# Kernel tuning notes

Measured on AMD Instinct MI355X. Metric: run time of the kernel, lower is better.

The kernel has to match this reference:

```python
import jax, jax.numpy as jnp
from jax import lax
import numpy as np

B, T, H, V, C = 64, 64, 1024, 32000, 10
Z, CD = 32, 8  # latent dim, cond embedding dim


def lstm_scan(x_tbh, h0, c0, Wih, Whh, bih, bhh):
    """PyTorch-convention LSTM over time. x_tbh: [T,B,H]; returns hs [T,B,H]."""
    def step(carry, x):
        h, c = carry
        gates = x @ Wih.T + bih + h @ Whh.T + bhh  # [B,4H]
        i, f, g, o = jnp.split(gates, 4, axis=-1)
        c = jax.nn.sigmoid(f) * c + jax.nn.sigmoid(i) * jnp.tanh(g)
        h = jax.nn.sigmoid(o) * jnp.tanh(c)
        return (h, c), h
    _, hs = lax.scan(step, (h0, c0), x_tbh)
    return hs


def setup_inputs() -> dict:
    key = jax.random.key(0)
    ks = jax.random.split(key, 24)
    s = 0.02
    d = {
        'input_word': jax.random.randint(ks[0], (B, T), 0, V),
        'cond': jax.random.randint(ks[1], (B,), 0, C),
        'emb_N': jax.random.normal(ks[2], (V, H), jnp.float32) * s,
        'Wih_N': jax.random.normal(ks[3], (4 * H, H), jnp.float32) * s,
        'Whh_N': jax.random.normal(ks[4], (4 * H, H), jnp.float32) * s,
        'bih_N': jnp.zeros((4 * H,), jnp.float32),
        'bhh_N': jnp.zeros((4 * H,), jnp.float32),
        'emb_D': jax.random.normal(ks[5], (V, H), jnp.float32) * s,
        'Wih_D': jax.random.normal(ks[6], (4 * H, H), jnp.float32) * s,
        'Whh_D': jax.random.normal(ks[7], (4 * H, H), jnp.float32) * s,
        'bih_D': jnp.zeros((4 * H,), jnp.float32),
        'bhh_D': jnp.zeros((4 * H,), jnp.float32),
        'emb_cond': jax.random.normal(ks[8], (C, CD), jnp.float32) * s,
        'W_mean': jax.random.normal(ks[9], (Z, H), jnp.float32) * s,
        'b_mean': jnp.zeros((Z,), jnp.float32),
        'W_logvar': jax.random.normal(ks[10], (Z, H), jnp.float32) * s,
        'b_logvar': jnp.zeros((Z,), jnp.float32),
        'W_st': jax.random.normal(ks[11], (H, Z + CD), jnp.float32) * s,
        'b_st': jnp.zeros((H,), jnp.float32),
        'W_out': jax.random.normal(ks[12], (V, H), jnp.float32) * s,
        'b_out': jnp.zeros((V,), jnp.float32),
        'eps': jax.random.normal(ks[13], (B, Z), jnp.float32),
    }
    return d


def reference(input_word, cond, emb_N, Wih_N, Whh_N, bih_N, bhh_N,
              emb_D, Wih_D, Whh_D, bih_D, bhh_D, emb_cond,
              W_mean, b_mean, W_logvar, b_logvar, W_st, b_st,
              W_out, b_out, eps):
    cond_e = emb_cond[cond]                              # [B,8]
    # ---- encoder ----
    x_enc = jnp.transpose(emb_N[input_word], (1, 0, 2))  # [T,B,H]
    h0 = jnp.concatenate([jnp.zeros((B, H - CD), x_enc.dtype), cond_e], axis=-1)
    c0 = jnp.zeros((B, H), x_enc.dtype)
    hs = lstm_scan(x_enc, h0, c0, Wih_N, Whh_N, bih_N, bhh_N)
    h_t = hs[-1]                                         # [B,H]
    mean_h = h_t @ W_mean.T + b_mean                     # [B,32]
    logvar_h = h_t @ W_logvar.T + b_logvar               # [B,32]
    latent_h = eps * jnp.exp(0.5 * logvar_h) + mean_h    # reparameterize
    # ---- decoder (teacher forcing, start token 0) ----
    hd0 = jnp.concatenate([latent_h, cond_e], axis=-1) @ W_st.T + b_st  # [B,H]
    cd0 = jnp.zeros((B, H), hd0.dtype)
    dec_tok = jnp.concatenate(
        [jnp.zeros((B, 1), input_word.dtype), input_word[:, :-1]], axis=1)
    x_dec = jnp.transpose(emb_D[dec_tok], (1, 0, 2))     # [T,B,H]
    hs_d = lstm_scan(x_dec, hd0, cd0, Wih_D, Whh_D, bih_D, bhh_D)  # [T,B,H]
    logits = hs_d @ W_out.T + b_out                      # [T,B,V]
    return jnp.transpose(logits, (1, 0, 2))              # [B,T,V]
```

## Files before the change

kernel.cpp:

```cpp
#include <hip/hip_runtime.h>
#include <hip/hip_bf16.h>

typedef unsigned short u16;
typedef unsigned int   u32;
typedef unsigned long long u64;
typedef __attribute__((ext_vector_type(8))) short short8;
typedef __attribute__((ext_vector_type(4))) float f32x4;

#define DEVINL static __device__ __forceinline__

DEVINL u16 f2bf(float x) {
  u32 u = __float_as_uint(x);
  u32 r = (u + 0x7fffu + ((u >> 16) & 1u)) >> 16;
  return (u16)r;
}

#define GLD16(gp, lp) __builtin_amdgcn_global_load_lds(                     \
    (const __attribute__((address_space(1))) u32*)(gp),                     \
    (__attribute__((address_space(3))) u32*)(lp), 16, 0, 0)

__global__ __launch_bounds__(256) void conv4(
    const float* __restrict__ s0, u16* __restrict__ d0,
    const float* __restrict__ s1, u16* __restrict__ d1,
    const float* __restrict__ s2, u16* __restrict__ d2,
    const float* __restrict__ s3, u16* __restrict__ d3) {
  int blk = blockIdx.x;
  int p = blk >> 12, local = blk & 4095;
  const float* s = (p == 0) ? s0 : (p == 1) ? s1 : (p == 2) ? s2 : s3;
  u16*         d = (p == 0) ? d0 : (p == 1) ? d1 : (p == 2) ? d2 : d3;
  int i = local * 256 + threadIdx.x;
  float4 v = ((const float4*)s)[i];
  ushort4 o;
  o.x = f2bf(v.x); o.y = f2bf(v.y); o.z = f2bf(v.z); o.w = f2bf(v.w);
  ((ushort4*)d)[i] = o;
}

__global__ __launch_bounds__(256) void conv_wout(const float* __restrict__ s,
                                                 u16* __restrict__ d) {
  int i = blockIdx.x * 256 + threadIdx.x;
  float4 v = ((const float4*)s)[i];
  ushort4 o;
  o.x = f2bf(v.x); o.y = f2bf(v.y); o.z = f2bf(v.z); o.w = f2bf(v.w);
  ((ushort4*)d)[i] = o;
}

__global__ __launch_bounds__(256) void prep_small(
    const int* __restrict__ cond, const float* __restrict__ emb_cond,
    const float* __restrict__ bihN, const float* __restrict__ bhhN,
    const float* __restrict__ bihD, const float* __restrict__ bhhD,
    float* __restrict__ ce, float* __restrict__ biasN, float* __restrict__ biasD,
    u32* __restrict__ bar) {
  int tid = blockIdx.x * 256 + threadIdx.x;
  if (tid < 512) {
    int b = tid >> 3, j = tid & 7;
    ce[tid] = emb_cond[cond[b] * 8 + j];
  }
  int i = tid - 512;
  if (i >= 0 && i < 4096) {
    biasN[i] = bihN[i] + bhhN[i];
    biasD[i] = bihD[i] + bhhD[i];
  }
  int k = tid - 4608;
  if (k >= 0 && k < 1024) bar[k] = 0;
}

__global__ __launch_bounds__(256) void init_enc(const float* __restrict__ ce,
                                                u16* __restrict__ hb0) {
  int tid = blockIdx.x * 256 + threadIdx.x;
  int b = tid >> 10, col = tid & 1023;
  float v = (col >= 1016) ? ce[b * 8 + (col - 1016)] : 0.f;
  hb0[tid] = f2bf(v);
}

__global__ __launch_bounds__(256) void gather_kernel(const float* __restrict__ emb,
                                                     const int* __restrict__ words,
                                                     u16* __restrict__ X, int dec) {
  int r = blockIdx.x;
  int t = r >> 6, b = r & 63;
  int tok = dec ? ((t == 0) ? 0 : words[b * 64 + t - 1]) : words[b * 64 + t];
  float4 v = ((const float4*)(emb + (size_t)tok * 1024))[threadIdx.x];
  ushort4 o;
  o.x = f2bf(v.x); o.y = f2bf(v.y); o.z = f2bf(v.z); o.w = f2bf(v.w);
  ((ushort4*)(X + (size_t)r * 1024))[threadIdx.x] = o;
}

DEVINL void gemm0_body(char* smemc, int bid, int nwg,
                       const u16* __restrict__ A, const u16* __restrict__ B,
                       float* __restrict__ C, const float* __restrict__ bias,
                       int N, int K) {
  u16 (*lA)[256 * 32] = (u16(*)[256 * 32])smemc;
  u16 (*lB)[128 * 32] = (u16(*)[128 * 32])(smemc + 32768);
  const int tid = threadIdx.x;
  const int lane = tid & 63;
  const int wid = tid >> 6;

  const int nn = N >> 7;
  const int wgid = (bid & 7) * (nwg >> 3) + (bid >> 3);
  const int tile_m = (wgid / nn) * 256;
  const int tile_n = (wgid % nn) * 128;
  const int wm = wid >> 1, wn = wid & 1;

  const int ldr = lane >> 2;
  const int lko = (lane & 3) * 8;
  const int l15 = lane & 15;
  const int g4 = lane >> 4;

  const size_t aBase = (size_t)tile_m * K;
  const size_t bBase = (size_t)tile_n * K;

  auto stage = [&](int buf, int k0) {
#pragma unroll
    for (int q = 0; q < 2; ++q) {
      int chk = wid * 2 + q;
      int row = chk * 16 + ldr;
      GLD16(A + aBase + (size_t)row * K + k0 + lko, &lA[buf][chk * 512]);
    }
    int row = wid * 16 + ldr;
    GLD16(B + bBase + (size_t)row * K + k0 + lko, &lB[buf][wid * 512]);
  };

  f32x4 acc[4][4];
#pragma unroll
  for (int i = 0; i < 4; ++i)
#pragma unroll
    for (int j = 0; j < 4; ++j) acc[i][j] = (f32x4)0.f;

  stage(0, 0);
  __syncthreads();

  const int NIT = K >> 5;
  for (int it = 0; it < NIT; ++it) {
    const int cur = it & 1;
    if (it + 1 < NIT) stage(cur ^ 1, (it + 1) * 32);
    short8 af[4], bf[4];
#pragma unroll
    for (int i = 0; i < 4; ++i)
      af[i] = *(const short8*)&lA[cur][(wm * 64 + i * 16 + l15) * 32 + g4 * 8];
#pragma unroll
    for (int j = 0; j < 4; ++j)
      bf[j] = *(const short8*)&lB[cur][(wn * 64 + j * 16 + l15) * 32 + g4 * 8];
#pragma unroll
    for (int i = 0; i < 4; ++i)
#pragma unroll
      for (int j = 0; j < 4; ++j)
        acc[i][j] = __builtin_amdgcn_mfma_f32_16x16x32_bf16(af[i], bf[j], acc[i][j], 0, 0, 0);
    __syncthreads();
  }

#pragma unroll
  for (int i = 0; i < 4; ++i) {
    int row0 = tile_m + wm * 64 + i * 16 + (g4 << 2);
#pragma unroll
    for (int j = 0; j < 4; ++j) {
      int col = tile_n + wn * 64 + j * 16 + l15;
      float bv = bias[col];
#pragma unroll
      for (int e = 0; e < 4; ++e)
        C[(size_t)(row0 + e) * (size_t)N + col] = acc[i][j][e] + bv;
    }
  }
}

DEVINL void lstm_body(char* smemc, const u16* __restrict__ Whh,
                      const float* __restrict__ Xp, u16* __restrict__ hbuf,
                      u16* __restrict__ hs_out, float* __restrict__ hT_out,
                      u32* arrive, u32* prog, int wgi) {
  char* smemA = smemc;
  float (*lg)[16][16] = (float(*)[16][16])(smemc + 32768);
  const int tid = threadIdx.x;
  const int lane = tid & 63;
  const int v = tid >> 6;
  const int gate = v >> 1;
  const int ch = v & 1;
  const int c = wgi >> 5;
  const int j = wgi & 31;
  const int b0 = c * 16, col0 = j * 32;
  const int l15 = lane & 15, g4 = lane >> 4;

  short8 breg[32];
  {
    const u16* Brow = Whh + (size_t)(gate * 1024 + col0 + ch * 16 + l15) * 1024
                          + g4 * 8;
#pragma unroll
    for (int kk = 0; kk < 32; ++kk)
      breg[kk] = *(const short8*)(Brow + kk * 32);
  }

  const int crow = tid >> 5, colw = tid & 31;
  const int bg = b0 + crow, cgl = col0 + colw;
  const int ch2 = colw >> 4, cw = colw & 15;
  float creg = 0.f;

  float xg0, xg1, xg2, xg3;
  {
    size_t xrow = (size_t)bg * 4096 + cgl;
    xg0 = __builtin_nontemporal_load(&Xp[xrow]);
    xg1 = __builtin_nontemporal_load(&Xp[xrow + 1024]);
    xg2 = __builtin_nontemporal_load(&Xp[xrow + 2048]);
    xg3 = __builtin_nontemporal_load(&Xp[xrow + 3072]);
  }

  for (int t = 0; t < 64; ++t) {
    const char* rbase = (const char*)(hbuf + (size_t)(t & 1) * 65536)
                      + (size_t)b0 * 2048;
    u32* wb32 = (u32*)(hbuf + (size_t)((t + 1) & 1) * 65536);

#pragma unroll
    for (int q = 0; q < 4; ++q) {
      int g = q * 512 + tid;
      int row = g >> 7;
      int cb = (g & 127) * 16;
      const u64* src = (const u64*)(rbase + (size_t)row * 2048 + cb);
      u64 lo = __hip_atomic_load(src,     __ATOMIC_RELAXED, __HIP_MEMORY_SCOPE_AGENT);
      u64 hi = __hip_atomic_load(src + 1, __ATOMIC_RELAXED, __HIP_MEMORY_SCOPE_AGENT);
      u64* d = (u64*)(smemA + row * 2048 + (cb ^ ((row & 7) << 4)));
      d[0] = lo; d[1] = hi;
    }
    __syncthreads();

    f32x4 a4[4] = {(f32x4)0.f, (f32x4)0.f, (f32x4)0.f, (f32x4)0.f};
#pragma unroll
    for (int kk = 0; kk < 32; ++kk) {
      int cb2 = kk * 64 + g4 * 16;
      const short8 a = *(const short8*)(smemA + l15 * 2048 + (cb2 ^ ((l15 & 7) << 4)));
      a4[kk & 3] = __builtin_amdgcn_mfma_f32_16x16x32_bf16(a, breg[kk], a4[kk & 3], 0, 0, 0);
    }
    f32x4 asum = a4[0] + a4[1] + a4[2] + a4[3];
    {
      int m = g4 * 4;
#pragma unroll
      for (int e = 0; e < 4; ++e) lg[v][m + e][l15] = asum[e];
    }
    __syncthreads();

    {
      float gi = lg[0 + ch2][crow][cw] + xg0;
      float gf = lg[2 + ch2][crow][cw] + xg1;
      float gg = lg[4 + ch2][crow][cw] + xg2;
      float go = lg[6 + ch2][crow][cw] + xg3;
      float si = 1.f / (1.f + __expf(-gi));
      float sf = 1.f / (1.f + __expf(-gf));
      float so = 1.f / (1.f + __expf(-go));
      float tg = tanhf(gg);
      float cn = sf * creg + si * tg;
      float hn = so * tanhf(cn);
      creg = cn;
      u16 h16 = f2bf(hn);
      u32 mine = h16;
      u32 other = (u32)__shfl_xor((int)mine, 1);
      if (!(colw & 1)) {
        u32 pk = mine | (other << 16);
        __hip_atomic_store(wb32 + (((size_t)bg * 1024 + cgl) >> 1), pk,
                           __ATOMIC_RELAXED, __HIP_MEMORY_SCOPE_AGENT);
        if (hs_out)
          __hip_atomic_store((u32*)hs_out + ((((size_t)t * 64 + bg) * 1024 + cgl) >> 1),
                             pk, __ATOMIC_RELAXED, __HIP_MEMORY_SCOPE_AGENT);
      }
      if (hT_out && t == 63) hT_out[bg * 1024 + cgl] = hn;
    }

    if (t != 63) {
      {
        size_t xrow = (size_t)((t + 1) * 64 + bg) * 4096 + cgl;
        xg0 = __builtin_nontemporal_load(&Xp[xrow]);
        xg1 = __builtin_nontemporal_load(&Xp[xrow + 1024]);
        xg2 = __builtin_nontemporal_load(&Xp[xrow + 2048]);
        xg3 = __builtin_nontemporal_load(&Xp[xrow + 3072]);
      }
      u32 want = (u32)(t + 1);
      asm volatile("s_waitcnt vmcnt(0)" ::: "memory");
      __syncthreads();
      if (tid == 0)
        __hip_atomic_store(&arrive[wgi], want, __ATOMIC_RELAXED,
                           __HIP_MEMORY_SCOPE_AGENT);
      if (tid < 32) {
        int guard = 0;
        while (__hip_atomic_load(&arrive[c * 32 + tid], __ATOMIC_RELAXED,
                                 __HIP_MEMORY_SCOPE_AGENT) < want) {
          __builtin_amdgcn_s_sleep(2);
          if (++guard > (1 << 20)) break;
        }
      }
      __syncthreads();
      if (prog && j == 0 && tid == 0)
        __hip_atomic_store(&prog[c], want, __ATOMIC_RELAXED,
                           __HIP_MEMORY_SCOPE_AGENT);
    }
  }

  if (prog) {
    asm volatile("s_waitcnt vmcnt(0)" ::: "memory");
    __syncthreads();
    if (tid == 0)
      __hip_atomic_store(&arrive[wgi], 64u, __ATOMIC_RELAXED,
                         __HIP_MEMORY_SCOPE_AGENT);
    if (j == 0) {
      if (tid < 32) {
        int guard = 0;
        while (__hip_atomic_load(&arrive[c * 32 + tid], __ATOMIC_RELAXED,
                                 __HIP_MEMORY_SCOPE_AGENT) < 64u) {
          __builtin_amdgcn_s_sleep(2);
          if (++guard > (1 << 20)) break;
        }
      }
      __syncthreads();
      if (tid == 0)
        __hip_atomic_store(&prog[c], 64u, __ATOMIC_RELAXED,
                           __HIP_MEMORY_SCOPE_AGENT);
    }
  }
}

__global__ __launch_bounds__(512, 1) void lstm_cluster(
    const u16* __restrict__ Whh, const float* __restrict__ Xp,
    u16* __restrict__ hbuf, float* __restrict__ hT_out, u32* arrive) {
  __shared__ __align__(16) char smem[40960];
  lstm_body(smem, Whh, Xp, hbuf, nullptr, hT_out, arrive, nullptr, blockIdx.x);
}

__global__ __launch_bounds__(512) void gemm_bt0(
    const u16* __restrict__ A, const u16* __restrict__ B,
    float* __restrict__ C, const float* __restrict__ bias, int N, int K) {
  __shared__ __align__(16) char smem[49152];
  gemm0_body(smem, blockIdx.x, gridDim.x, A, B, C, bias, N, K);
}

__global__ __launch_bounds__(512, 1) void enc_fused(
    const u16* __restrict__ whhN, const float* __restrict__ XpE,
    u16* __restrict__ hbuf, float* __restrict__ hT_out, u32* arrive,
    const u16* __restrict__ Xd, const u16* __restrict__ wihD,
    float* __restrict__ XpD, const float* __restrict__ biasD,
    const float* __restrict__ Wout, u16* __restrict__ wout) {
  __shared__ __align__(16) char smem[49152];
  if (blockIdx.x < 128) {
    lstm_body(smem, whhN, XpE, hbuf, nullptr, hT_out, arrive, nullptr, blockIdx.x);
  } else if (blockIdx.x < 640) {
    gemm0_body(smem, blockIdx.x - 128, 512, Xd, wihD, XpD, biasD, 4096, 1024);
  } else {
    int tid0 = (blockIdx.x - 640) * 512 + threadIdx.x;
    for (int i = tid0; i < 8192000; i += 512 * 512) {
      float4 v = ((const float4*)Wout)[i];
      ushort4 o;
      o.x = f2bf(v.x); o.y = f2bf(v.y); o.z = f2bf(v.z); o.w = f2bf(v.w);
      ((ushort4*)wout)[i] = o;
    }
  }
}

__global__ __launch_bounds__(512, 1) void dec_fused(
    const u16* __restrict__ whhD, const float* __restrict__ XpD,
    u16* __restrict__ hbuf, u16* __restrict__ hsd, u32* arrive, u32* prog,
    const u16* __restrict__ wout, float* __restrict__ out,
    const float* __restrict__ b_out) {
  __shared__ __align__(16) char smem[49152];
  if (blockIdx.x < 128) {
    lstm_body(smem, whhD, XpD, hbuf, hsd, nullptr, arrive, prog, blockIdx.x);
    return;
  }
  u16 (*lA)[256 * 32] = (u16(*)[256 * 32])smem;
  u16 (*lB)[128 * 32] = (u16(*)[128 * 32])(smem + 32768);
  const int tid = threadIdx.x;
  const int lane = tid & 63;
  const int wid = tid >> 6;

  const int i = blockIdx.x - 128;
  const int x = i & 7;
  const int k = i >> 3;
  const int mg = k >> 6;
  const int r  = k & 63;
  const int kn = r >> 1;
  const int mi = r & 1;
  const int tn = kn * 8 + x;
  if (tn >= 250) return;
  const int mt = mg * 2 + mi;
  const int tile_m = mt * 256;
  const int tile_n = tn * 128;
  const int wm = wid >> 1, wn = wid & 1;
  const int N = 32000, K = 1024;

  {
    u32 need = (u32)(mt * 4 + 4);
    if (tid < 4) {
      int guard = 0;
      while (__hip_atomic_load(&prog[tid], __ATOMIC_RELAXED,
                               __HIP_MEMORY_SCOPE_AGENT) < need) {
        __builtin_amdgcn_s_sleep(8);
        if (++guard > (1 << 22)) break;
      }
    }
    __syncthreads();
  }

  const int ldr = lane >> 2;
  const int lko = (lane & 3) * 8;
  const int l15 = lane & 15;
  const int g4 = lane >> 4;

  const size_t aBase = (size_t)tile_m * K;
  const size_t bBase = (size_t)tile_n * K;

  f32x4 acc[4][4];
#pragma unroll
  for (int i2 = 0; i2 < 4; ++i2)
#pragma unroll
    for (int j2 = 0; j2 < 4; ++j2) acc[i2][j2] = (f32x4)0.f;

  auto stg = [&](int buf, int k0) {
#pragma unroll
    for (int q = 0; q < 2; ++q) {
      int chk = wid * 2 + q;
      int row = chk * 16 + ldr;
      GLD16(hsd + aBase + (size_t)row * K + k0 + lko, &lA[buf][chk * 512]);
    }
    int row = wid * 16 + ldr;
    GLD16(wout + bBase + (size_t)row * K + k0 + lko, &lB[buf][wid * 512]);
  };

  stg(0, 0);
  __syncthreads();

  const int NIT = K >> 5;
  for (int it = 0; it < NIT; ++it) {
    const int cur = it & 1;
    if (it + 1 < NIT) stg(cur ^ 1, (it + 1) * 32);
    short8 af[4], bf[4];
#pragma unroll
    for (int i2 = 0; i2 < 4; ++i2)
      af[i2] = *(const short8*)&lA[cur][(wm * 64 + i2 * 16 + l15) * 32 + g4 * 8];
#pragma unroll
    for (int j2 = 0; j2 < 4; ++j2)
      bf[j2] = *(const short8*)&lB[cur][(wn * 64 + j2 * 16 + l15) * 32 + g4 * 8];
#pragma unroll
    for (int i2 = 0; i2 < 4; ++i2)
#pragma unroll
      for (int j2 = 0; j2 < 4; ++j2)
        acc[i2][j2] = __builtin_amdgcn_mfma_f32_16x16x32_bf16(af[i2], bf[j2], acc[i2][j2], 0, 0, 0);
    __syncthreads();
  }

#pragma unroll
  for (int i2 = 0; i2 < 4; ++i2) {
    int row0 = tile_m + wm * 64 + i2 * 16 + (g4 << 2);
#pragma unroll
    for (int j2 = 0; j2 < 4; ++j2) {
      int col = tile_n + wn * 64 + j2 * 16 + l15;
      float bv = b_out[col];
#pragma unroll
      for (int e = 0; e < 4; ++e) {
        int rr = row0 + e;
        size_t o = (size_t)((rr & 63) * 64 + (rr >> 6)) * (size_t)N + col;
        __builtin_nontemporal_store(acc[i2][j2][e] + bv, &out[o]);
      }
    }
  }
}

__global__ __launch_bounds__(256) void latent_hd0_kernel(
    const float* hT, const float* Wm, const float* bm,
    const float* Wl, const float* bl, const float* Wst, const float* bst,
    const float* eps, const float* ce, u16* hb0) {
  __shared__ float red[64][4];
  __shared__ float ml[64];
  __shared__ float lat[40];
  int b = blockIdx.x;
  int tid = threadIdx.x;
  int o = tid >> 2, p = tid & 3;
  const float* w = (o < 32) ? (Wm + (size_t)o * 1024) : (Wl + (size_t)(o - 32) * 1024);
  const float* h = hT + (size_t)b * 1024;
  float s = 0.f;
  for (int k = p * 256; k < p * 256 + 256; ++k) s += h[k] * w[k];
  red[o][p] = s;
  __syncthreads();
  if (tid < 64) {
    float v = red[tid][0] + red[tid][1] + red[tid][2] + red[tid][3];
    v += (tid < 32) ? bm[tid] : bl[tid - 32];
    ml[tid] = v;
  }
  __syncthreads();
  if (tid < 32) lat[tid] = eps[b * 32 + tid] * __expf(0.5f * ml[32 + tid]) + ml[tid];
  if (tid >= 32 && tid < 40) lat[tid] = ce[b * 8 + (tid - 32)];
  __syncthreads();
  for (int hc = tid; hc < 1024; hc += 256) {
    float s2 = bst[hc];
    const float* wr = Wst + (size_t)hc * 40;
#pragma unroll
    for (int j = 0; j < 40; ++j) s2 += lat[j] * wr[j];
    hb0[b * 1024 + hc] = f2bf(s2);
  }
}

extern "C" void kernel_launch(void* const* d_in, const int* in_sizes, int n_in,
                              void* d_out, int out_size, void* d_ws, size_t ws_size,
                              hipStream_t stream) {
  const int*   input_word = (const int*)d_in[0];
  const int*   cond       = (const int*)d_in[1];
  const float* emb_N      = (const float*)d_in[2];
  const float* Wih_N      = (const float*)d_in[3];
  const float* Whh_N      = (const float*)d_in[4];
  const float* bih_N      = (const float*)d_in[5];
  const float* bhh_N      = (const float*)d_in[6];
  const float* emb_D      = (const float*)d_in[7];
  const float* Wih_D      = (const float*)d_in[8];
  const float* Whh_D      = (const float*)d_in[9];
  const float* bih_D      = (const float*)d_in[10];
  const float* bhh_D      = (const float*)d_in[11];
  const float* emb_cond   = (const float*)d_in[12];
  const float* W_mean     = (const float*)d_in[13];
  const float* b_mean     = (const float*)d_in[14];
  const float* W_logvar   = (const float*)d_in[15];
  const float* b_logvar   = (const float*)d_in[16];
  const float* W_st       = (const float*)d_in[17];
  const float* b_st       = (const float*)d_in[18];
  const float* W_out      = (const float*)d_in[19];
  const float* b_out      = (const float*)d_in[20];
  const float* eps        = (const float*)d_in[21];
  float* out = (float*)d_out;

  char* ws = (char*)d_ws;
  size_t off = 0;
  auto alloc = [&](size_t b) { size_t p = off; off += (b + 255) & ~(size_t)255; return p; };
  u16*   wihN = (u16*)(ws + alloc(4096ull * 1024 * 2));
  u16*   whhN = (u16*)(ws + alloc(4096ull * 1024 * 2));
  u16*   wihD = (u16*)(ws + alloc(4096ull * 1024 * 2));
  u16*   whhD = (u16*)(ws + alloc(4096ull * 1024 * 2));
  u16*   wout = (u16*)(ws + alloc(32000ull * 1024 * 2));
  u16*   Xe   = (u16*)(ws + alloc(4096ull * 1024 * 2));
  u16*   Xd   = (u16*)(ws + alloc(4096ull * 1024 * 2));
  float* Xp   = (float*)(ws + alloc(4096ull * 4096 * 4));
  u16*   hsd  = (u16*)(ws + alloc(4096ull * 1024 * 2));
  u16*   hb   = (u16*)(ws + alloc(2ull * 64 * 1024 * 2));
  float* hf   = (float*)(ws + alloc(64ull * 1024 * 4));
  float* biasN = (float*)(ws + alloc(4096 * 4));
  float* biasD = (float*)(ws + alloc(4096 * 4));
  float* ce    = (float*)(ws + alloc(64 * 8 * 4));
  u32*   bar   = (u32*)(ws + alloc(4096));
  size_t base_off = off;
  float* XpD2 = (float*)(ws + alloc(4096ull * 4096 * 4));
  if (base_off > ws_size) return;
  const bool fused = (off <= ws_size);
  float* XpD = fused ? XpD2 : Xp;

  conv4<<<16384, 256, 0, stream>>>(Wih_N, wihN, Whh_N, whhN,
                                   Wih_D, wihD, Whh_D, whhD);
  prep_small<<<22, 256, 0, stream>>>(cond, emb_cond, bih_N, bhh_N, bih_D, bhh_D,
                                     ce, biasN, biasD, bar);
  gather_kernel<<<4096, 256, 0, stream>>>(emb_N, input_word, Xe, 0);
  gather_kernel<<<4096, 256, 0, stream>>>(emb_D, input_word, Xd, 1);
  init_enc<<<256, 256, 0, stream>>>(ce, hb);

  gemm_bt0<<<512, 512, 0, stream>>>(Xe, wihN, Xp, biasN, 4096, 1024);
  if (fused) {
    enc_fused<<<1152, 512, 0, stream>>>(whhN, Xp, hb, hf, bar + 0,
                                        Xd, wihD, XpD, biasD, W_out, wout);
  } else {
    conv_wout<<<32000, 256, 0, stream>>>(W_out, wout);
    lstm_cluster<<<128, 512, 0, stream>>>(whhN, Xp, hb, hf, bar + 0);
  }
  latent_hd0_kernel<<<64, 256, 0, stream>>>(hf, W_mean, b_mean, W_logvar, b_logvar,
                                            W_st, b_st, eps, ce, hb);
  if (!fused)
    gemm_bt0<<<512, 512, 0, stream>>>(Xd, wihD, XpD, biasD, 4096, 1024);
  dec_fused<<<4224, 512, 0, stream>>>(whhD, XpD, hb, hsd, bar + 256, bar + 512,
                                      wout, out, b_out);
}
```

Before: 998.2 us.

## Split decoder LSTM and output projection into separate sequential kernels

Removes the fused decoder kernel in which output-projection GEMM blocks spun on per-timestep progress flags written by the LSTM blocks. The decoder LSTM now runs as a standalone 128-block cluster kernel writing hidden states, followed by a separate GEMM launch for the logits. This drops the progress-flag signalling and the spinning blocks that competed with the recurrent loop for compute units. In exchange it gives up overlapping the vocabulary projection with the recurrence.

```diff
diff --git a/kernel.cpp b/kernel.cpp
--- a/kernel.cpp
+++ b/kernel.cpp
@@ -164,7 +164,7 @@
 DEVINL void lstm_body(char* smemc, const u16* __restrict__ Whh,
                       const float* __restrict__ Xp, u16* __restrict__ hbuf,
                       u16* __restrict__ hs_out, float* __restrict__ hT_out,
-                      u32* arrive, u32* prog, int wgi) {
+                      u32* arrive, int wgi) {
   char* smemA = smemc;
   float (*lg)[16][16] = (float(*)[16][16])(smemc + 32768);
   const int tid = threadIdx.x;
@@ -282,40 +282,16 @@
         }
       }
       __syncthreads();
-      if (prog && j == 0 && tid == 0)
-        __hip_atomic_store(&prog[c], want, __ATOMIC_RELAXED,
-                           __HIP_MEMORY_SCOPE_AGENT);
-    }
-  }
-
-  if (prog) {
-    asm volatile("s_waitcnt vmcnt(0)" ::: "memory");
-    __syncthreads();
-    if (tid == 0)
-      __hip_atomic_store(&arrive[wgi], 64u, __ATOMIC_RELAXED,
-                         __HIP_MEMORY_SCOPE_AGENT);
-    if (j == 0) {
-      if (tid < 32) {
-        int guard = 0;
-        while (__hip_atomic_load(&arrive[c * 32 + tid], __ATOMIC_RELAXED,
-                                 __HIP_MEMORY_SCOPE_AGENT) < 64u) {
-          __builtin_amdgcn_s_sleep(2);
-          if (++guard > (1 << 20)) break;
-        }
-      }
-      __syncthreads();
-      if (tid == 0)
-        __hip_atomic_store(&prog[c], 64u, __ATOMIC_RELAXED,
-                           __HIP_MEMORY_SCOPE_AGENT);
     }
   }
 }
 
 __global__ __launch_bounds__(512, 1) void lstm_cluster(
     const u16* __restrict__ Whh, const float* __restrict__ Xp,
-    u16* __restrict__ hbuf, float* __restrict__ hT_out, u32* arrive) {
+    u16* __restrict__ hbuf, u16* __restrict__ hs_out,
+    float* __restrict__ hT_out, u32* arrive) {
   __shared__ __align__(16) char smem[40960];
-  lstm_body(smem, Whh, Xp, hbuf, nullptr, hT_out, arrive, nullptr, blockIdx.x);
+  lstm_body(smem, Whh, Xp, hbuf, hs_out, hT_out, arrive, blockIdx.x);
 }
 
 __global__ __launch_bounds__(512) void gemm_bt0(
@@ -333,7 +309,7 @@
     const float* __restrict__ Wout, u16* __restrict__ wout) {
   __shared__ __align__(16) char smem[49152];
   if (blockIdx.x < 128) {
-    lstm_body(smem, whhN, XpE, hbuf, nullptr, hT_out, arrive, nullptr, blockIdx.x);
+    lstm_body(smem, whhN, XpE, hbuf, nullptr, hT_out, arrive, blockIdx.x);
   } else if (blockIdx.x < 640) {
     gemm0_body(smem, blockIdx.x - 128, 512, Xd, wihD, XpD, biasD, 4096, 1024);
   } else {
@@ -347,23 +323,16 @@
   }
 }
 
-__global__ __launch_bounds__(512, 1) void dec_fused(
-    const u16* __restrict__ whhD, const float* __restrict__ XpD,
-    u16* __restrict__ hbuf, u16* __restrict__ hsd, u32* arrive, u32* prog,
-    const u16* __restrict__ wout, float* __restrict__ out,
-    const float* __restrict__ b_out) {
-  __shared__ __align__(16) char smem[49152];
-  if (blockIdx.x < 128) {
-    lstm_body(smem, whhD, XpD, hbuf, hsd, nullptr, arrive, prog, blockIdx.x);
-    return;
-  }
-  u16 (*lA)[256 * 32] = (u16(*)[256 * 32])smem;
-  u16 (*lB)[128 * 32] = (u16(*)[128 * 32])(smem + 32768);
+__global__ __launch_bounds__(512) void gemm_bt1(
+    const u16* __restrict__ hsd, const u16* __restrict__ wout,
+    float* __restrict__ out, const float* __restrict__ b_out) {
+  __shared__ u16 lA[2][256 * 32];
+  __shared__ u16 lB[2][128 * 32];
   const int tid = threadIdx.x;
   const int lane = tid & 63;
   const int wid = tid >> 6;
 
-  const int i = blockIdx.x - 128;
+  const int i = blockIdx.x;
   const int x = i & 7;
   const int k = i >> 3;
   const int mg = k >> 6;
@@ -372,24 +341,10 @@
   const int mi = r & 1;
   const int tn = kn * 8 + x;
   if (tn >= 250) return;
-  const int mt = mg * 2 + mi;
-  const int tile_m = mt * 256;
+  const int tile_m = (mg * 2 + mi) * 256;
   const int tile_n = tn * 128;
   const int wm = wid >> 1, wn = wid & 1;
   const int N = 32000, K = 1024;
-
-  {
-    u32 need = (u32)(mt * 4 + 4);
-    if (tid < 4) {
-      int guard = 0;
-      while (__hip_atomic_load(&prog[tid], __ATOMIC_RELAXED,
-                               __HIP_MEMORY_SCOPE_AGENT) < need) {
-        __builtin_amdgcn_s_sleep(8);
-        if (++guard > (1 << 22)) break;
-      }
-    }
-    __syncthreads();
-  }
 
   const int ldr = lane >> 2;
   const int lko = (lane & 3) * 8;
@@ -399,12 +354,6 @@
   const size_t aBase = (size_t)tile_m * K;
   const size_t bBase = (size_t)tile_n * K;
 
-  f32x4 acc[4][4];
-#pragma unroll
-  for (int i2 = 0; i2 < 4; ++i2)
-#pragma unroll
-    for (int j2 = 0; j2 < 4; ++j2) acc[i2][j2] = (f32x4)0.f;
-
   auto stg = [&](int buf, int k0) {
 #pragma unroll
     for (int q = 0; q < 2; ++q) {
@@ -415,6 +364,12 @@
     int row = wid * 16 + ldr;
     GLD16(wout + bBase + (size_t)row * K + k0 + lko, &lB[buf][wid * 512]);
   };
+
+  f32x4 acc[4][4];
+#pragma unroll
+  for (int i2 = 0; i2 < 4; ++i2)
+#pragma unroll
+    for (int j2 = 0; j2 < 4; ++j2) acc[i2][j2] = (f32x4)0.f;
 
   stg(0, 0);
   __syncthreads();
@@ -554,12 +509,12 @@
                                         Xd, wihD, XpD, biasD, W_out, wout);
   } else {
     conv_wout<<<32000, 256, 0, stream>>>(W_out, wout);
-    lstm_cluster<<<128, 512, 0, stream>>>(whhN, Xp, hb, hf, bar + 0);
+    lstm_cluster<<<128, 512, 0, stream>>>(whhN, Xp, hb, nullptr, hf, bar + 0);
   }
   latent_hd0_kernel<<<64, 256, 0, stream>>>(hf, W_mean, b_mean, W_logvar, b_logvar,
                                             W_st, b_st, eps, ce, hb);
   if (!fused)
     gemm_bt0<<<512, 512, 0, stream>>>(Xd, wihD, XpD, biasD, 4096, 1024);
-  dec_fused<<<4224, 512, 0, stream>>>(whhD, XpD, hb, hsd, bar + 256, bar + 512,
-                                      wout, out, b_out);
-}
+  lstm_cluster<<<128, 512, 0, stream>>>(whhD, XpD, hb, hsd, nullptr, bar + 256);
+  gemm_bt1<<<4096, 512, 0, stream>>>(hsd, wout, out, b_out);
+}
```

Measured after the change: 1.038 ms. 3.9% more time.
